# Kernel tuning notes

Measured on AMD Instinct MI355X. Metric: run time of the kernel, lower is better.

Reference implementation:

```python
import jax, jax.numpy as jnp
import numpy as np

N_NODES = 20000
N_EDGES = 320000
N_FEAT = 128
N_CLASS = 10
NEG_SLOPE = 0.2  # PyG GATConv default LeakyReLU slope


def gat_conv(x, src, dst, ew, W, a_src, a_dst, b, heads, ch, concat):
    """PyG-style GATConv with multiplicative edge_weight on messages.
    x: [N, Fin]; src/dst: [E] (self-loops already included); ew: [E].
    """
    N = x.shape[0]
    h = (x @ W).reshape(N, heads, ch)                      # [N,H,C]
    al_s = jnp.sum(h * a_src, axis=-1)                     # [N,H]
    al_d = jnp.sum(h * a_dst, axis=-1)                     # [N,H]
    e = jax.nn.leaky_relu(al_s[src] + al_d[dst], NEG_SLOPE)  # [E,H]
    # segment softmax over incoming edges of each target node
    m = jax.ops.segment_max(e, dst, num_segments=N)        # [N,H]
    ex = jnp.exp(e - m[dst])
    den = jax.ops.segment_sum(ex, dst, num_segments=N)     # [N,H]
    alpha = ex / (den[dst] + 1e-16)                        # [E,H]
    msg = h[src] * (alpha * ew[:, None])[..., None]        # [E,H,C]
    out = jax.ops.segment_sum(msg, dst, num_segments=N)    # [N,H,C]
    out = out.reshape(N, heads * ch) if concat else out.mean(axis=1)
    return out + b


def setup_inputs() -> dict:
    key = jax.random.key(0)
    ks = jax.random.split(key, 20)
    d = {}
    d["x"] = jax.random.normal(ks[0], (N_NODES, N_FEAT), dtype=jnp.float32)
    d["edge_index"] = jax.random.randint(ks[1], (2, N_EDGES), 0, N_NODES, dtype=jnp.int32)
    d["edge_weight"] = jnp.ones((N_EDGES,), dtype=jnp.float32)

    def glorot(k, shape):
        fan = shape[0] + shape[-1]
        return jax.random.uniform(k, shape, jnp.float32, -1.0, 1.0) * np.sqrt(6.0 / fan)

    H1, C1 = 4, 256
    H3, C3 = 6, N_CLASS
    d["W1"] = glorot(ks[2], (N_FEAT, H1 * C1))
    d["a1s"] = glorot(ks[3], (H1, C1)) * 0.1
    d["a1d"] = glorot(ks[4], (H1, C1)) * 0.1
    d["b1"] = jnp.zeros((H1 * C1,), jnp.float32)
    d["lw1"] = glorot(ks[5], (N_FEAT, H1 * C1))
    d["lb1"] = jnp.zeros((H1 * C1,), jnp.float32)

    d["W2"] = glorot(ks[6], (H1 * C1, H1 * C1))
    d["a2s"] = glorot(ks[7], (H1, C1)) * 0.1
    d["a2d"] = glorot(ks[8], (H1, C1)) * 0.1
    d["b2"] = jnp.zeros((H1 * C1,), jnp.float32)
    d["lw2"] = glorot(ks[9], (H1 * C1, H1 * C1))
    d["lb2"] = jnp.zeros((H1 * C1,), jnp.float32)

    d["W3"] = glorot(ks[10], (H1 * C1, H3 * C3))
    d["a3s"] = glorot(ks[11], (H3, C3)) * 0.1
    d["a3d"] = glorot(ks[12], (H3, C3)) * 0.1
    d["b3"] = jnp.zeros((C3,), jnp.float32)
    d["lw3"] = glorot(ks[13], (H1 * C1, C3))
    d["lb3"] = jnp.zeros((C3,), jnp.float32)
    return d


def reference(x, edge_index, edge_weight,
              W1, a1s, a1d, b1, lw1, lb1,
              W2, a2s, a2d, b2, lw2, lb2,
              W3, a3s, a3d, b3, lw3, lb3):
    N = x.shape[0]
    # PyG GATConv adds self-loops (fill edge_weight with 1.0)
    loop = jnp.arange(N, dtype=edge_index.dtype)
    src = jnp.concatenate([edge_index[0], loop])
    dst = jnp.concatenate([edge_index[1], loop])
    ew = jnp.concatenate([edge_weight, jnp.ones((N,), edge_weight.dtype)])

    h = jax.nn.elu(gat_conv(x, src, dst, ew, W1, a1s, a1d, b1, 4, 256, True)
                   + (x @ lw1 + lb1))
    h = jax.nn.elu(gat_conv(h, src, dst, ew, W2, a2s, a2d, b2, 4, 256, True)
                   + (h @ lw2 + lb2))
    out = gat_conv(h, src, dst, ew, W3, a3s, a3d, b3, 6, N_CLASS, False) \
          + (h @ lw3 + lb3)
    return out
```

## Files before the change

### kernel.cpp

```cpp
#include <hip/hip_runtime.h>

typedef __attribute__((ext_vector_type(8))) short s16x8;
typedef __attribute__((ext_vector_type(8))) __bf16 bf16x8;
typedef __attribute__((ext_vector_type(4))) float f32x4;

__device__ inline float bf2f(ushort u){ return __uint_as_float(((unsigned)u)<<16); }
__device__ inline ushort f2bf(float f){
  unsigned u = __float_as_uint(f);
  unsigned r = (u + 0x7fffu + ((u>>16)&1u)) >> 16;
  return (ushort)r;
}

__device__ inline void gl_lds16(const ushort* g, ushort* l){
  __builtin_amdgcn_global_load_lds(
      (const __attribute__((address_space(1))) unsigned int*)g,
      (__attribute__((address_space(3))) unsigned int*)l,
      16, 0, 0);
}

__global__ void k_count(const int* __restrict__ ei, int* __restrict__ counts,
                        int E, int ET){
  int e = blockIdx.x*256 + threadIdx.x;
  if (e >= ET) return;
  int dst = (e < E) ? ei[E + e] : (e - E);
  atomicAdd(&counts[dst], 1);
}

__global__ __launch_bounds__(1024) void k_scan(const int* __restrict__ cnt,
                                               int* __restrict__ indptr, int N){
  __shared__ int part[1024];
  int t = threadIdx.x;
  int per = (N + 1023) / 1024;
  int base = t * per;
  int s = 0;
  for (int i = 0; i < per; ++i){ int idx = base + i; if (idx < N) s += cnt[idx]; }
  part[t] = s; __syncthreads();
  for (int off = 1; off < 1024; off <<= 1){
    int v = (t >= off) ? part[t-off] : 0;
    __syncthreads();
    if (t >= off) part[t] += v;
    __syncthreads();
  }
  int run = (t == 0) ? 0 : part[t-1];
  for (int i = 0; i < per; ++i){
    int idx = base + i;
    if (idx < N){ indptr[idx] = run; run += cnt[idx]; }
  }
  if (t == 1023) indptr[N] = run;
}

__global__ void k_fill(const int* __restrict__ ei, const float* __restrict__ ew,
                       const int* __restrict__ indptr, int* __restrict__ cursor,
                       int* __restrict__ csrc, float* __restrict__ cew,
                       int E, int ET){
  int e = blockIdx.x*256 + threadIdx.x;
  if (e >= ET) return;
  int src, dst; float w;
  if (e < E){ src = ei[e]; dst = ei[E + e]; w = ew[e]; }
  else { src = dst = e - E; w = 1.0f; }
  int pos = indptr[dst] + atomicAdd(&cursor[dst], 1);
  csrc[pos] = src; cew[pos] = w;
}

__global__ void k_f2b(const float* __restrict__ x, ushort* __restrict__ xb,
                      int n8valid, int n8total){
  int i = blockIdx.x*256 + threadIdx.x;
  if (i >= n8total) return;
  s16x8 o = {0,0,0,0,0,0,0,0};
  if (i < n8valid){
    const float4* p = (const float4*)x + (size_t)i*2;
    float4 a = p[0], b = p[1];
    o[0]=(short)f2bf(a.x); o[1]=(short)f2bf(a.y); o[2]=(short)f2bf(a.z); o[3]=(short)f2bf(a.w);
    o[4]=(short)f2bf(b.x); o[5]=(short)f2bf(b.y); o[6]=(short)f2bf(b.z); o[7]=(short)f2bf(b.w);
  }
  *((s16x8*)xb + i) = o;
}

__global__ __launch_bounds__(256) void k_packB(
    const float* __restrict__ W, const float* __restrict__ LW,
    ushort* __restrict__ BT, int K, int NW, int NL, int Npad)
{
  __shared__ float tile[32][33];
  int k0 = blockIdx.x*32, n0 = blockIdx.y*32;
  int c = threadIdx.x & 31, r4 = threadIdx.x >> 5;
  #pragma unroll
  for (int rr = 0; rr < 32; rr += 8){
    int k = k0 + r4 + rr, n = n0 + c;
    float v = 0.f;
    if (k < K){
      if (n < NW)            v = W[(size_t)k*NW + n];
      else if (n < NW + NL)  v = LW[(size_t)k*NL + (n - NW)];
    }
    tile[r4+rr][c] = v;
  }
  __syncthreads();
  #pragma unroll
  for (int rr = 0; rr < 32; rr += 8){
    int n = n0 + r4 + rr, k = k0 + c;
    if (n < Npad && k < K) BT[(size_t)n*K + k] = f2bf(tile[c][r4+rr]);
  }
}

__global__ __launch_bounds__(256) void k_gemm(
    const ushort* __restrict__ A, const ushort* __restrict__ BT,
    ushort* __restrict__ Gatt, ushort* __restrict__ Skip,
    int K, int GW, int SW, int NCB, int CPX)
{
  __shared__ ushort As[128*64];
  __shared__ ushort Bs[128*64];
  const int bid = blockIdx.x;
  const int lb = CPX ? ((bid & 7)*CPX + (bid >> 3)) : bid;
  const size_t row0 = (size_t)(lb / NCB) * 128;
  const size_t col0 = (size_t)(lb % NCB) * 128;
  const int t = threadIdx.x;
  const int l = t & 63, w = t >> 6;
  const int wr = w >> 1, wc = w & 1;
  const int sr = l >> 3;
  const int sk = ((l & 7) ^ sr) << 3;
  const ushort* gA = A  + (row0 + w*8 + sr)*(size_t)K + sk;
  const ushort* gB = BT + (col0 + w*8 + sr)*(size_t)K + sk;
  ushort* lA = As + w*512;
  ushort* lB = Bs + w*512;
  const int rf = l & 15;
  const int g4 = l >> 4;
  f32x4 acc[4][4] = {};

  for (int k0 = 0; k0 < K; k0 += 64){
    #pragma unroll
    for (int i = 0; i < 4; ++i){
      gl_lds16(gA + k0 + (size_t)(i*32)*K, lA + i*2048);
      gl_lds16(gB + k0 + (size_t)(i*32)*K, lB + i*2048);
    }
    __syncthreads();
    #pragma unroll
    for (int kk = 0; kk < 2; ++kk){
      const int koff = ((((kk<<2) | g4) ^ (rf & 7)) << 3);
      bf16x8 af[4], bfr[4];
      #pragma unroll
      for (int i = 0; i < 4; ++i)
        af[i] = __builtin_bit_cast(bf16x8, *(const s16x8*)(As + (wr*64 + i*16 + rf)*64 + koff));
      #pragma unroll
      for (int j = 0; j < 4; ++j)
        bfr[j] = __builtin_bit_cast(bf16x8, *(const s16x8*)(Bs + (wc*64 + j*16 + rf)*64 + koff));
      #pragma unroll
      for (int i = 0; i < 4; ++i)
        #pragma unroll
        for (int j = 0; j < 4; ++j)
          acc[i][j] = __builtin_amdgcn_mfma_f32_16x16x32_bf16(af[i], bfr[j], acc[i][j], 0, 0, 0);
    }
    __syncthreads();
  }

  #pragma unroll
  for (int i = 0; i < 4; ++i){
    #pragma unroll
    for (int j = 0; j < 4; ++j){
      int gc = (int)col0 + wc*64 + j*16 + rf;
      #pragma unroll
      for (int r = 0; r < 4; ++r){
        size_t gr = row0 + wr*64 + i*16 + (g4<<2) + r;
        float v = acc[i][j][r];
        if (gc < GW)            Gatt[gr*GW + gc] = f2bf(v);
        else if (gc < GW + SW)  Skip[gr*SW + (gc - GW)] = f2bf(v);
      }
    }
  }
}

__global__ __launch_bounds__(256) void k_al(const ushort* __restrict__ Gatt,
    const float* __restrict__ a_s, const float* __restrict__ a_d,
    float* __restrict__ als, float* __restrict__ ald, int N){
  int gw = (blockIdx.x*blockDim.x + threadIdx.x) >> 6;
  int l = threadIdx.x & 63;
  if (gw >= N) return;
  const ushort* row = Gatt + (size_t)gw*1024;
  int c0 = l*16;
  s16x8 v0 = *(const s16x8*)(row + c0);
  s16x8 v1 = *(const s16x8*)(row + c0 + 8);
  float ps = 0.f, pd = 0.f;
  #pragma unroll
  for (int q = 0; q < 8; ++q){
    float f0 = bf2f((ushort)v0[q]), f1 = bf2f((ushort)v1[q]);
    ps += f0*a_s[c0+q] + f1*a_s[c0+8+q];
    pd += f0*a_d[c0+q] + f1*a_d[c0+8+q];
  }
  #pragma unroll
  for (int off = 8; off; off >>= 1){
    ps += __shfl_down(ps, off);
    pd += __shfl_down(pd, off);
  }
  if ((l & 15) == 0){
    als[(size_t)gw*4 + (l>>4)] = ps;
    ald[(size_t)gw*4 + (l>>4)] = pd;
  }
}

__global__ __launch_bounds__(256) void k_agg(
    const ushort* __restrict__ Gatt,
    const ushort* __restrict__ Skip,
    const float*  __restrict__ als,
    const float*  __restrict__ ald,
    const float*  __restrict__ bias,
    const float*  __restrict__ lbias,
    const int*    __restrict__ indptr,
    const int*    __restrict__ csrc,
    const float*  __restrict__ cew,
    ushort* __restrict__ Hout,
    int N)
{
  const int n = blockIdx.x;
  const int t = threadIdx.x;
  if (n >= N){
    ushort4 z = {0,0,0,0};
    *(ushort4*)(Hout + (size_t)n*1024 + t*4) = z;
    return;
  }
  const int l = t & 63, w = t >> 6;
  const int beg = indptr[n];
  const int deg = indptr[n+1] - beg;
  __shared__ float s_ald[4], s_m[4], s_den[4];
  __shared__ int   s_src[64];
  __shared__ float s_w[64][4];
  __shared__ float s_part[3][64][16];
  if (t < 4) s_ald[t] = ald[(size_t)n*4 + t];
  __syncthreads();
  const bool fast = (deg <= 64);

  if (fast){
    int e2 = t >> 2, hh = t & 3;
    if (e2 < deg){
      int s = csrc[beg + e2];
      if (hh == 0) s_src[e2] = s;
      float r_ = als[(size_t)s*4 + hh] + s_ald[hh];
      s_w[e2][hh] = r_ > 0.f ? r_ : 0.2f*r_;
    }
    __syncthreads();
    float mye = (l < deg) ? s_w[l][w] : -1e30f;
    float mx = mye;
    #pragma unroll
    for (int o = 32; o; o >>= 1) mx = fmaxf(mx, __shfl_xor(mx, o));
    float ex = (l < deg) ? __expf(mye - mx) : 0.f;
    float den = ex;
    #pragma unroll
    for (int o = 32; o; o >>= 1) den += __shfl_xor(den, o);
    den += 1e-16f;
    if (l < deg) s_w[l][w] = ex / den * cew[beg + l];
    __syncthreads();
  } else {
    const float aldh = s_ald[w];
    float mx = -1e30f;
    for (int i = l; i < deg; i += 64){
      int s = csrc[beg+i];
      float e = als[(size_t)s*4 + w] + aldh;
      e = e > 0.f ? e : 0.2f*e;
      mx = fmaxf(mx, e);
    }
    #pragma unroll
    for (int off = 32; off; off >>= 1) mx = fmaxf(mx, __shfl_xor(mx, off));
    if (l == 0) s_m[w] = mx;
    __syncthreads();
    const float mh = s_m[w];
    float den = 0.f;
    for (int i = l; i < deg; i += 64){
      int s = csrc[beg+i];
      float e = als[(size_t)s*4 + w] + aldh;
      e = e > 0.f ? e : 0.2f*e;
      den += __expf(e - mh);
    }
    #pragma unroll
    for (int off = 32; off; off >>= 1) den += __shfl_xor(den, off);
    if (l == 0) s_den[w] = den + 1e-16f;
    __syncthreads();
  }

  const int h2 = l >> 4;
  const ushort* gbase = Gatt + (size_t)l*16;
  float a[16];
  #pragma unroll
  for (int q = 0; q < 16; ++q) a[q] = 0.f;
  for (int c0 = 0; c0 < deg; c0 += 64){
    int nc = min(64, deg - c0);
    if (!fast){
      int ei2 = t >> 2, hh = t & 3;
      if (ei2 < nc){
        int s = csrc[beg + c0 + ei2];
        if (hh == 0) s_src[ei2] = s;
        float e = als[(size_t)s*4 + hh] + s_ald[hh];
        e = e > 0.f ? e : 0.2f*e;
        s_w[ei2][hh] = __expf(e - s_m[hh]) / s_den[hh] * cew[beg + c0 + ei2];
      }
      __syncthreads();
    }
    for (int j = w; j < nc; j += 4){
      int s = s_src[j];
      float wg = s_w[j][h2];
      const ushort* rp = gbase + (size_t)s*1024;
      s16x8 h0 = *(const s16x8*)rp;
      s16x8 h1 = *(const s16x8*)(rp + 8);
      #pragma unroll
      for (int q = 0; q < 8; ++q) a[q] += wg * bf2f((ushort)h0[q]);
      #pragma unroll
      for (int q = 0; q < 8; ++q) a[q+8] += wg * bf2f((ushort)h1[q]);
    }
    __syncthreads();
  }
  if (w){
    #pragma unroll
    for (int q = 0; q < 16; ++q) s_part[w-1][l][q] = a[q];
  }
  __syncthreads();
  if (w == 0){
    #pragma unroll
    for (int q = 0; q < 16; ++q) a[q] += s_part[0][l][q] + s_part[1][l][q] + s_part[2][l][q];
    const int col = l*16;
    s16x8 sk0 = *(const s16x8*)(Skip + (size_t)n*1024 + col);
    s16x8 sk1 = *(const s16x8*)(Skip + (size_t)n*1024 + col + 8);
    s16x8 ov0, ov1;
    #pragma unroll
    for (int q = 0; q < 8; ++q){
      float v = a[q] + bias[col+q] + lbias[col+q] + bf2f((ushort)sk0[q]);
      v = v > 0.f ? v : __expf(v) - 1.f;
      ov0[q] = (short)f2bf(v);
      float v2 = a[q+8] + bias[col+8+q] + lbias[col+8+q] + bf2f((ushort)sk1[q]);
      v2 = v2 > 0.f ? v2 : __expf(v2) - 1.f;
      ov1[q] = (short)f2bf(v2);
    }
    *(s16x8*)(Hout + (size_t)n*1024 + col)     = ov0;
    *(s16x8*)(Hout + (size_t)n*1024 + col + 8) = ov1;
  }
}

__global__ void k_al3(const ushort* __restrict__ G3, const float* __restrict__ a_s,
                      const float* __restrict__ a_d,
                      float* __restrict__ als, float* __restrict__ ald, int N){
  int n = blockIdx.x*256 + threadIdx.x;
  if (n >= N) return;
  const ushort* row = G3 + (size_t)n*60;
  #pragma unroll
  for (int h = 0; h < 6; ++h){
    float ps = 0.f, pd = 0.f;
    #pragma unroll
    for (int c = 0; c < 10; ++c){
      float v = bf2f(row[h*10 + c]);
      ps += v * a_s[h*10 + c];
      pd += v * a_d[h*10 + c];
    }
    als[(size_t)n*6 + h] = ps;
    ald[(size_t)n*6 + h] = pd;
  }
}

__global__ __launch_bounds__(64) void k_agg3(
    const ushort* __restrict__ G3,
    const ushort* __restrict__ Skip3,
    const float*  __restrict__ als,
    const float*  __restrict__ ald,
    const float*  __restrict__ b3,
    const float*  __restrict__ lb3,
    const int*    __restrict__ indptr,
    const int*    __restrict__ csrc,
    const float*  __restrict__ cew,
    float* __restrict__ out, int N)
{
  const int n = blockIdx.x;
  const int l = threadIdx.x;
  const int beg = indptr[n], deg = indptr[n+1] - beg;
  __shared__ float s_aldh[6];
  __shared__ int   s_src[64];
  __shared__ float s_wgt[64][6];
  __shared__ float s_o[6][10];
  if (l < 6) s_aldh[l] = ald[(size_t)n*6 + l];
  __syncthreads();
  float m0=-1e30f,m1=-1e30f,m2=-1e30f,m3=-1e30f,m4=-1e30f,m5=-1e30f;
  float d0=0.f,d1=0.f,d2=0.f,d3=0.f,d4=0.f,d5=0.f;
  for (int c0 = 0; c0 < deg; c0 += 64){
    int nc = min(64, deg - c0);
    bool act = l < nc;
    int s = act ? csrc[beg + c0 + l] : 0;
#define HP(hh, mm, dd) { \
    float e = -1e30f; \
    if (act){ float r_ = als[(size_t)s*6 + hh] + s_aldh[hh]; e = r_ > 0.f ? r_ : 0.2f*r_; } \
    float cm = e; \
    for (int o_ = 32; o_; o_ >>= 1) cm = fmaxf(cm, __shfl_xor(cm, o_)); \
    float nm = fmaxf(mm, cm); \
    float ex = act ? __expf(e - nm) : 0.f; \
    for (int o_ = 32; o_; o_ >>= 1) ex += __shfl_xor(ex, o_); \
    dd = dd * __expf(mm - nm) + ex; mm = nm; }
    HP(0,m0,d0) HP(1,m1,d1) HP(2,m2,d2) HP(3,m3,d3) HP(4,m4,d4) HP(5,m5,d5)
#undef HP
  }
  const int h = l / 10, c = l % 10;
  float o = 0.f;
  for (int c0 = 0; c0 < deg; c0 += 64){
    int nc = min(64, deg - c0);
    if (l < nc){
      int s = csrc[beg + c0 + l];
      s_src[l] = s;
      float w_ = cew[beg + c0 + l];
#define WP(hh, mm, dd) { \
      float r_ = als[(size_t)s*6 + hh] + s_aldh[hh]; \
      float e = r_ > 0.f ? r_ : 0.2f*r_; \
      s_wgt[l][hh] = __expf(e - mm) / (dd + 1e-16f) * w_; }
      WP(0,m0,d0) WP(1,m1,d1) WP(2,m2,d2) WP(3,m3,d3) WP(4,m4,d4) WP(5,m5,d5)
#undef WP
    }
    __syncthreads();
    if (l < 60){
      for (int i = 0; i < nc; ++i)
        o += s_wgt[i][h] * bf2f(G3[(size_t)s_src[i]*60 + l]);
    }
    __syncthreads();
  }
  if (l < 60) s_o[h][c] = o;
  __syncthreads();
  if (l < 10){
    float v = (s_o[0][l]+s_o[1][l]+s_o[2][l]+s_o[3][l]+s_o[4][l]+s_o[5][l]) * (1.0f/6.0f);
    v += b3[l] + lb3[l] + bf2f(Skip3[(size_t)n*10 + l]);
    out[(size_t)n*10 + l] = v;
  }
}

extern "C" void kernel_launch(void* const* d_in, const int* in_sizes, int n_in,
                              void* d_out, int out_size, void* d_ws, size_t ws_size,
                              hipStream_t stream)
{
  const int N = 20000, F = 128, E = 320000, ET = E + N;
  const int Mpad = 20096;
  const int F1 = 1024, NT = 2048;
  const int NWG = (Mpad/128)*(NT/128);

  const float* x   = (const float*)d_in[0];
  const int*   ei  = (const int*)  d_in[1];
  const float* ew  = (const float*)d_in[2];
  const float* W1  = (const float*)d_in[3];
  const float* a1s = (const float*)d_in[4];
  const float* a1d = (const float*)d_in[5];
  const float* b1  = (const float*)d_in[6];
  const float* lw1 = (const float*)d_in[7];
  const float* lb1 = (const float*)d_in[8];
  const float* W2  = (const float*)d_in[9];
  const float* a2s = (const float*)d_in[10];
  const float* a2d = (const float*)d_in[11];
  const float* b2  = (const float*)d_in[12];
  const float* lw2 = (const float*)d_in[13];
  const float* lb2 = (const float*)d_in[14];
  const float* W3  = (const float*)d_in[15];
  const float* a3s = (const float*)d_in[16];
  const float* a3d = (const float*)d_in[17];
  const float* b3  = (const float*)d_in[18];
  const float* lw3 = (const float*)d_in[19];
  const float* lb3 = (const float*)d_in[20];

  char* ws = (char*)d_ws;
  size_t off = 0;
  auto alloc = [&](size_t bytes) -> void* {
    void* p = ws + off;
    off = (off + bytes + 255) & ~(size_t)255;
    return p;
  };
  ushort* Gatt = (ushort*)alloc((size_t)Mpad*F1*2);
  ushort* Skip = (ushort*)alloc((size_t)Mpad*F1*2);
  ushort* H    = (ushort*)alloc((size_t)Mpad*F1*2);
  ushort* xb   = (ushort*)alloc((size_t)Mpad*F*2);
  ushort* BT   = (ushort*)alloc((size_t)NT*1024*2);
  float*  als  = (float*) alloc((size_t)N*6*4);
  float*  ald  = (float*) alloc((size_t)N*6*4);
  int*    counts = (int*)alloc((size_t)2*N*4);
  int*    cursor = counts + N;
  int*    indptr = (int*)alloc((size_t)(N+1)*4);
  int*    csrc   = (int*)alloc((size_t)ET*4);
  float*  cew    = (float*)alloc((size_t)ET*4);
  if (off > ws_size) return;

  hipMemsetAsync(counts, 0, (size_t)2*N*4, stream);
  k_count<<<(ET+255)/256, 256, 0, stream>>>(ei, counts, E, ET);
  k_scan<<<1, 1024, 0, stream>>>(counts, indptr, N);
  k_fill<<<(ET+255)/256, 256, 0, stream>>>(ei, ew, indptr, cursor, csrc, cew, E, ET);
  k_f2b<<<(Mpad*F/8+255)/256, 256, 0, stream>>>(x, xb, N*F/8, Mpad*F/8);

  k_packB<<<dim3((F+31)/32, NT/32), 256, 0, stream>>>(W1, lw1, BT, F, 1024, 1024, NT);
  k_gemm<<<dim3(NWG), 256, 0, stream>>>(xb, BT, Gatt, Skip, F, 1024, 1024, NT/128, NWG/8);
  k_al<<<(N+3)/4, 256, 0, stream>>>(Gatt, a1s, a1d, als, ald, N);
  k_agg<<<Mpad, 256, 0, stream>>>(Gatt, Skip, als, ald, b1, lb1, indptr, csrc, cew, H, N);

  k_packB<<<dim3(F1/32, NT/32), 256, 0, stream>>>(W2, lw2, BT, F1, 1024, 1024, NT);
  k_gemm<<<dim3(NWG), 256, 0, stream>>>(H, BT, Gatt, Skip, F1, 1024, 1024, NT/128, NWG/8);
  k_al<<<(N+3)/4, 256, 0, stream>>>(Gatt, a2s, a2d, als, ald, N);
  k_agg<<<Mpad, 256, 0, stream>>>(Gatt, Skip, als, ald, b2, lb2, indptr, csrc, cew, H, N);

  k_packB<<<dim3(F1/32, 128/32), 256, 0, stream>>>(W3, lw3, BT, F1, 60, 10, 128);
  k_gemm<<<dim3(Mpad/128), 256, 0, stream>>>(H, BT, Gatt, Skip, F1, 60, 10, 1, 0);
  k_al3<<<(N+255)/256, 256, 0, stream>>>(Gatt, a3s, a3d, als, ald, N);
  k_agg3<<<N, 64, 0, stream>>>(Gatt, Skip, als, ald, b3, lb3, indptr, csrc, cew,
                               (float*)d_out, N);
}
```

Measured before the change: 501.3 us.

## Add 256x256-tile 8-wave pipelined GEMM for layer-2 projection

Adds a new GEMM kernel for the large layer-2 projection (K=1024, N=2048). It uses 512 threads, 256x256 output tiles, double-buffered LDS loaded directly from global memory with XOR swizzling, four sub-phases that interleave MFMA with prefetch, and setprio hints. The larger tiles are meant to cut global traffic per FLOP and hide load latency. In exchange, row padding grows to a multiple of 256, which raises the work in the padded rows, and the full 128KB of LDS per block leaves one block per CU.

```diff
diff --git a/kernel.cpp b/kernel.cpp
--- a/kernel.cpp
+++ b/kernel.cpp
@@ -165,6 +165,109 @@
       }
     }
   }
+}
+
+#define STG8(p0, hh, ktv, offU) do { \
+  const ushort* _g = (p0) + (((size_t)(hh))<<7)*(size_t)K + (((size_t)(ktv))<<6); \
+  gl_lds16(_g, S + (offU) + (w<<9)); \
+  gl_lds16(_g + ((size_t)K<<6), S + (offU) + 4096 + (w<<9)); \
+} while(0)
+
+#define PHASE8(bb, mh, nh, ...) do { \
+  const ushort* Ab = S + (bb)*32768 + (mh)*8192; \
+  const ushort* Bb = S + (bb)*32768 + 16384 + (nh)*8192; \
+  bf16x8 av[4][2], bv[2][2]; \
+  _Pragma("unroll") \
+  for (int i_ = 0; i_ < 4; ++i_){ \
+    const int hr = wr*64 + i_*16 + rf; \
+    const int sw = hr & 7; \
+    av[i_][0] = *(const bf16x8*)(Ab + hr*64 + ((g4 ^ sw) << 3)); \
+    av[i_][1] = *(const bf16x8*)(Ab + hr*64 + (((4|g4) ^ sw) << 3)); } \
+  _Pragma("unroll") \
+  for (int j_ = 0; j_ < 2; ++j_){ \
+    const int cf = wc*32 + j_*16 + rf; \
+    const int sw = cf & 7; \
+    bv[j_][0] = *(const bf16x8*)(Bb + cf*64 + ((g4 ^ sw) << 3)); \
+    bv[j_][1] = *(const bf16x8*)(Bb + cf*64 + (((4|g4) ^ sw) << 3)); } \
+  __VA_ARGS__; \
+  asm volatile("s_barrier" ::: "memory"); \
+  __builtin_amdgcn_s_setprio(1); \
+  _Pragma("unroll") \
+  for (int kk_ = 0; kk_ < 2; ++kk_) \
+    _Pragma("unroll") \
+    for (int i_ = 0; i_ < 4; ++i_) \
+      _Pragma("unroll") \
+      for (int j_ = 0; j_ < 2; ++j_) \
+        acc[mh][nh][i_][j_] = __builtin_amdgcn_mfma_f32_16x16x32_bf16( \
+            av[i_][kk_], bv[j_][kk_], acc[mh][nh][i_][j_], 0, 0, 0); \
+  __builtin_amdgcn_s_setprio(0); \
+} while(0)
+
+__global__ __launch_bounds__(512, 1) void k_gemm8(
+    const ushort* __restrict__ A, const ushort* __restrict__ BT,
+    ushort* __restrict__ Gatt, ushort* __restrict__ Skip,
+    int K, int GW, int CPX)
+{
+  __shared__ ushort S[65536];
+  const int bid = blockIdx.x;
+  const int lb = (bid & 7)*CPX + (bid >> 3);
+  const size_t row0 = (size_t)(lb >> 3) * 256;
+  const size_t col0 = (size_t)(lb & 7) * 256;
+  const int t = threadIdx.x;
+  const int l = t & 63, w = t >> 6;
+  const int wr = w >> 2, wc = w & 3;
+  const int rf = l & 15, g4 = l >> 4;
+  const int T = K >> 6;
+
+  const int r0 = t >> 3, s0 = t & 7;
+  const ushort* pA = A  + (row0 + r0)*(size_t)K + ((s0 ^ (r0 & 7)) << 3);
+  const ushort* pB = BT + (col0 + r0)*(size_t)K + ((s0 ^ (r0 & 7)) << 3);
+
+  f32x4 acc[2][2][4][2] = {};
+
+  STG8(pA, 0, 0, 0);
+  STG8(pB, 0, 0, 16384);
+  STG8(pA, 1, 0, 8192);
+  STG8(pB, 1, 0, 24576);
+  STG8(pA, 0, 1, 32768);
+  STG8(pB, 0, 1, 49152);
+  asm volatile("s_waitcnt vmcnt(4)");
+  asm volatile("s_barrier" ::: "memory");
+
+  for (int u = 0; u < T; ++u){
+    const int b = u & 1;
+    const int bbase = b << 15;
+    const int nbase = bbase ^ 32768;
+    const bool un1 = (u + 1 < T), un2 = (u + 2 < T);
+    PHASE8(b, 0, 0, if (un1) STG8(pA, 1, u+1, nbase + 8192));
+    asm volatile("s_barrier" ::: "memory");
+    PHASE8(b, 0, 1, if (un1) STG8(pB, 1, u+1, nbase + 24576));
+    asm volatile("s_barrier" ::: "memory");
+    PHASE8(b, 1, 0, if (un2) STG8(pA, 0, u+2, bbase));
+    asm volatile("s_barrier" ::: "memory");
+    PHASE8(b, 1, 1, if (un2) STG8(pB, 0, u+2, bbase + 16384));
+    if (un2) asm volatile("s_waitcnt vmcnt(4)");
+    else     asm volatile("s_waitcnt vmcnt(0)");
+    asm volatile("s_barrier" ::: "memory");
+  }
+
+  ushort* outp; int cb;
+  if ((int)col0 < GW){ outp = Gatt; cb = (int)col0; }
+  else               { outp = Skip; cb = (int)col0 - GW; }
+  #pragma unroll
+  for (int mh = 0; mh < 2; ++mh)
+    #pragma unroll
+    for (int i = 0; i < 4; ++i)
+      #pragma unroll
+      for (int rr = 0; rr < 4; ++rr){
+        size_t gr = row0 + mh*128 + wr*64 + i*16 + (g4<<2) + rr;
+        ushort* rp = outp + gr*1024 + cb;
+        #pragma unroll
+        for (int nh = 0; nh < 2; ++nh)
+          #pragma unroll
+          for (int j = 0; j < 2; ++j)
+            rp[nh*128 + wc*32 + j*16 + rf] = f2bf(acc[mh][nh][i][j][rr]);
+      }
 }
 
 __global__ __launch_bounds__(256) void k_al(const ushort* __restrict__ Gatt,
@@ -425,9 +528,10 @@
                               hipStream_t stream)
 {
   const int N = 20000, F = 128, E = 320000, ET = E + N;
-  const int Mpad = 20096;
+  const int Mpad = 20224;
   const int F1 = 1024, NT = 2048;
-  const int NWG = (Mpad/128)*(NT/128);
+  const int NWG1 = (Mpad/128)*(NT/128);
+  const int NWG2 = (Mpad/256)*(NT/256);
 
   const float* x   = (const float*)d_in[0];
   const int*   ei  = (const int*)  d_in[1];
@@ -479,12 +583,12 @@
   k_f2b<<<(Mpad*F/8+255)/256, 256, 0, stream>>>(x, xb, N*F/8, Mpad*F/8);
 
   k_packB<<<dim3((F+31)/32, NT/32), 256, 0, stream>>>(W1, lw1, BT, F, 1024, 1024, NT);
-  k_gemm<<<dim3(NWG), 256, 0, stream>>>(xb, BT, Gatt, Skip, F, 1024, 1024, NT/128, NWG/8);
+  k_gemm<<<dim3(NWG1), 256, 0, stream>>>(xb, BT, Gatt, Skip, F, 1024, 1024, NT/128, NWG1/8);
   k_al<<<(N+3)/4, 256, 0, stream>>>(Gatt, a1s, a1d, als, ald, N);
   k_agg<<<Mpad, 256, 0, stream>>>(Gatt, Skip, als, ald, b1, lb1, indptr, csrc, cew, H, N);
 
   k_packB<<<dim3(F1/32, NT/32), 256, 0, stream>>>(W2, lw2, BT, F1, 1024, 1024, NT);
-  k_gemm<<<dim3(NWG), 256, 0, stream>>>(H, BT, Gatt, Skip, F1, 1024, 1024, NT/128, NWG/8);
+  k_gemm8<<<dim3(NWG2), 512, 0, stream>>>(H, BT, Gatt, Skip, F1, 1024, NWG2/8);
   k_al<<<(N+3)/4, 256, 0, stream>>>(Gatt, a2s, a2d, als, ald, N);
   k_agg<<<Mpad, 256, 0, stream>>>(Gatt, Skip, als, ald, b2, lb2, indptr, csrc, cew, H, N);
 
```

Measured after the change: 517.9 us. 3.3% more time.
